# Kernel tuning notes

Measured on AMD Instinct MI355X. Metric: run time of the kernel, lower is better.

The kernel has to match this reference:

```python
import jax, jax.numpy as jnp
import numpy as np

B, C, J, L = 8, 256, 16, 256
NB_CODE = 8192
S_SCALES = [1, 2, 4, 8, 16]
T_SCALES = [4, 16, 64, 128, 256]
PHI_IDX = [0, 1, 1, 2, 3]   # si/(SN-1) mapped onto PhiPartiallyShared ticks (K=4)
RESI = 0.5                  # quant_resi
BETA = 1.0


def setup_inputs() -> dict:
    key = jax.random.key(0)
    k1, k2, k3 = jax.random.split(key, 3)
    return {
        "f_bcjl": jax.random.normal(k1, (B, C, J, L), jnp.float32),
        "codebook": jax.random.normal(k2, (NB_CODE, C), jnp.float32),
        "phi_w": jax.random.normal(k3, (4, C, C, 3, 3), jnp.float32) * (1.0 / np.sqrt(C * 9)),
        "phi_b": jnp.zeros((4, C), jnp.float32),
    }


def _area_down(x, sn, tn):
    # F.interpolate(mode='area') with divisible sizes == mean pooling
    b, c, j, l = x.shape
    return x.reshape(b, c, sn, j // sn, tn, l // tn).mean(axis=(3, 5))


def _cubic_w(x, a=-0.75):
    # PyTorch bicubic kernel (a = -0.75)
    ax = jnp.abs(x)
    w1 = ((a + 2.0) * ax - (a + 3.0)) * ax * ax + 1.0
    w2 = a * (ax * ((ax - 5.0) * ax + 8.0) - 4.0)
    return jnp.where(ax <= 1.0, w1, jnp.where(ax < 2.0, w2, 0.0))


def _resize_cubic_axis(x, out_size, axis):
    x = jnp.moveaxis(x, axis, -1)
    n = x.shape[-1]
    scale = n / out_size
    coords = (jnp.arange(out_size, dtype=jnp.float32) + 0.5) * scale - 0.5
    i0 = jnp.floor(coords)
    t = coords - i0
    offs = jnp.arange(-1, 3)
    idx = jnp.clip(i0.astype(jnp.int32)[:, None] + offs, 0, n - 1)   # [out,4], border-clamped
    w = _cubic_w(t[:, None] - offs.astype(jnp.float32))              # [out,4]
    g = x[..., idx]                                                  # [...,out,4]
    y = jnp.einsum('...ok,ok->...o', g, w)
    return jnp.moveaxis(y, -1, axis)


def _up_bicubic(x, j, l):
    return _resize_cubic_axis(_resize_cubic_axis(x, j, 2), l, 3)


def _phi(h, w, b):
    y = jax.lax.conv_general_dilated(h, w, (1, 1), ((1, 1), (1, 1)),
                                     dimension_numbers=('NCHW', 'OIHW', 'NCHW'))
    y = y + b[None, :, None, None]
    return h * (1.0 - RESI) + y * RESI


def _forward(f, cb, pw, pb):
    f_ng = jax.lax.stop_gradient(f)
    f_rest = f_ng
    f_hat = jnp.zeros_like(f_ng)
    loss = jnp.float32(0.0)
    idx_all = []
    SN = len(S_SCALES)
    cb_sq = jnp.sum(cb * cb, axis=1)  # [nb_code]
    for si, (sn, tn) in enumerate(zip(S_SCALES, T_SCALES)):
        r = f_rest if si == SN - 1 else _area_down(f_rest, sn, tn)
        rest = r.transpose(0, 2, 3, 1).reshape(-1, C)                     # [N,C]
        d = jnp.sum(rest * rest, axis=1, keepdims=True) + cb_sq - 2.0 * (rest @ cb.T)
        idx = jnp.argmin(d, axis=-1)                                      # eval-mode gumbel_sample == argmax(-d)
        idx_all.append(idx)
        h = cb[idx].reshape(-1, sn, tn, C).transpose(0, 3, 1, 2)          # [B,C,sn,tn]
        if si != SN - 1:
            h = _up_bicubic(h, J, L)
        h = _phi(h, pw[PHI_IDX[si]], pb[PHI_IDX[si]])
        f_hat = f_hat + h
        f_rest = f_rest - h
        loss = loss + BETA * jnp.mean((jax.lax.stop_gradient(f_hat) - f) ** 2)
    loss = loss / SN
    f_hat_out = f_hat - f_ng + f   # straight-through estimator
    return f_hat_out, loss, jnp.concatenate(idx_all)


def _perplexity(idx):
    counts = jnp.zeros((NB_CODE,), jnp.float32).at[idx].add(1.0)
    prob = counts / jnp.sum(counts)
    return jnp.exp(-jnp.sum(prob * jnp.log(prob + 1e-7)))


def reference(f_bcjl, codebook, phi_w, phi_b):
    f_hat, loss, idx = _forward(f_bcjl, codebook, phi_w, phi_b)
    return f_hat, loss, _perplexity(idx)
```

## Files before the change

### kernel.cpp

```cpp
#include <hip/hip_runtime.h>
#include <stdint.h>

#define BB 8
#define CC 256
#define JJ 16
#define LL 256
#define NPIX 32768
#define NEL (BB*CC*JJ*LL)
#define NBC 8192
#define NTOT 43296

typedef unsigned short u16;
typedef short short8 __attribute__((ext_vector_type(8)));
typedef float floatx4 __attribute__((ext_vector_type(4)));

__device__ __forceinline__ uint32_t ord_f32(float f) {
  uint32_t u = __float_as_uint(f);
  return (u & 0x80000000u) ? ~u : (u | 0x80000000u);
}

__device__ __forceinline__ float cubw(float x) {
  const float a = -0.75f;
  float ax = fabsf(x);
  if (ax <= 1.f) return ((a + 2.f) * ax - (a + 3.f)) * ax * ax + 1.f;
  if (ax < 2.f)  return a * (ax * ((ax - 5.f) * ax + 8.f) - 4.f);
  return 0.f;
}

__device__ __forceinline__ u16 bf16h(float x) {
  uint32_t u = __float_as_uint(x);
  return (u16)((u + 0x7FFFu + ((u >> 16) & 1u)) >> 16);
}
__device__ __forceinline__ float bf16f(u16 h) {
  return __uint_as_float(((uint32_t)h) << 16);
}

__global__ void k_init(unsigned long long* __restrict__ bkey,
                       uint32_t* __restrict__ counts, float* __restrict__ lacc) {
  int i = blockIdx.x * 256 + threadIdx.x;
  int stride = gridDim.x * 256;
  for (int x = i; x < NTOT; x += stride) bkey[x] = 0xFFFFFFFFFFFFFFFFull;
  for (int x = i; x < NBC; x += stride) counts[x] = 0u;
  if (i < 8) lacc[i] = 0.f;
}

__global__ void k_f2pm(const float* __restrict__ f, float* __restrict__ pm) {
  __shared__ float t[64][65];
  int tid = threadIdx.x;
  int px0 = blockIdx.x * 64, c0 = blockIdx.y * 64;
  int b = px0 >> 12, y = (px0 >> 8) & 15, x0 = px0 & 255;
#pragma unroll
  for (int it = 0; it < 4; ++it) {
    int slot = it * 256 + tid;
    int c = slot >> 4, q = (slot & 15) * 4;
    float4 v = *(const float4*)(f + (((size_t)(b * 256 + c0 + c)) * 16 + y) * 256 + x0 + q);
    t[c][q] = v.x; t[c][q + 1] = v.y; t[c][q + 2] = v.z; t[c][q + 3] = v.w;
  }
  __syncthreads();
#pragma unroll
  for (int it = 0; it < 4; ++it) {
    int slot = it * 256 + tid;
    int i = slot >> 4, q = (slot & 15) * 4;
    float4 v;
    v.x = t[q + 0][i]; v.y = t[q + 1][i]; v.z = t[q + 2][i]; v.w = t[q + 3][i];
    *(float4*)(pm + (size_t)(px0 + i) * 256 + c0 + q) = v;
  }
}

__global__ void k_out(const float* __restrict__ f, const float* __restrict__ pm,
                      float* __restrict__ out) {
  __shared__ float t[64][65];
  int tid = threadIdx.x;
  int px0 = blockIdx.x * 64, c0 = blockIdx.y * 64;
  int b = px0 >> 12, y = (px0 >> 8) & 15, x0 = px0 & 255;
#pragma unroll
  for (int it = 0; it < 4; ++it) {
    int slot = it * 256 + tid;
    int i = slot >> 4, q = (slot & 15) * 4;
    float4 v = *(const float4*)(pm + (size_t)(px0 + i) * 256 + c0 + q);
    t[q + 0][i] = v.x; t[q + 1][i] = v.y; t[q + 2][i] = v.z; t[q + 3][i] = v.w;
  }
  __syncthreads();
#pragma unroll
  for (int it = 0; it < 4; ++it) {
    int slot = it * 256 + tid;
    int c = slot >> 4, q = (slot & 15) * 4;
    size_t g = (((size_t)(b * 256 + c0 + c)) * 16 + y) * 256 + x0 + q;
    float4 fv = *(const float4*)(f + g);
    float4 o;
    o.x = fv.x - t[c][q + 0]; o.y = fv.y - t[c][q + 1];
    o.z = fv.z - t[c][q + 2]; o.w = fv.w - t[c][q + 3];
    *(float4*)(out + g) = o;
  }
}

__global__ void k_cbsq(const float* __restrict__ cb, float* __restrict__ cbsq) {
  int k = blockIdx.x * blockDim.x + threadIdx.x;
  if (k >= NBC) return;
  const float4* row = (const float4*)(cb + (size_t)k * CC);
  float s = 0.f;
  for (int i = 0; i < CC / 4; ++i) {
    float4 v = row[i];
    s += v.x * v.x + v.y * v.y + v.z * v.z + v.w * v.w;
  }
  cbsq[k] = s;
}

__global__ void k_split(const float* __restrict__ src, u16* __restrict__ hi,
                        u16* __restrict__ lo, int n) {
  int i = (blockIdx.x * 256 + threadIdx.x) * 4;
  if (i >= n) return;
  float4 v = *(const float4*)(src + i);
  ushort4 h, l;
  h.x = bf16h(v.x); l.x = bf16h(v.x - bf16f(h.x));
  h.y = bf16h(v.y); l.y = bf16h(v.y - bf16f(h.y));
  h.z = bf16h(v.z); l.z = bf16h(v.z - bf16f(h.z));
  h.w = bf16h(v.w); l.w = bf16h(v.w - bf16f(h.w));
  *(ushort4*)(hi + i) = h;
  *(ushort4*)(lo + i) = l;
}

__global__ void k_wprep(const float* __restrict__ pw, u16* __restrict__ Whi,
                        u16* __restrict__ Wlo) {
  int bx = blockIdx.x;
  int co = bx & 255;
  int ps = bx >> 8;
  int phi = ps / 9, s = ps % 9;
  int ci = threadIdx.x;
  float v = pw[(((size_t)(phi * 256 + co)) * 256 + ci) * 9 + s];
  u16 h = bf16h(v);
  Whi[(size_t)bx * 256 + ci] = h;
  Wlo[(size_t)bx * 256 + ci] = bf16h(v - bf16f(h));
}

__global__ void k_poolpart(const float* __restrict__ pm, float* __restrict__ part,
                           int sn, int tn, int pj, int wl, int K, int ppk) {
  int n = blockIdx.x, kk = blockIdx.y, c = threadIdx.x;
  int b = n / (sn * tn);
  int s = (n / tn) % sn;
  int t = n % tn;
  float acc = 0.f;
  for (int q = kk * ppk; q < (kk + 1) * ppk; ++q) {
    int yy = s * pj + q / wl;
    int xx = t * wl + q % wl;
    size_t p = (size_t)b * 4096 + (size_t)yy * 256 + xx;
    acc += pm[p * 256 + c];
  }
  part[((size_t)n * K + kk) * 256 + c] = acc;
}

__global__ void k_poolfin(const float* __restrict__ part, float* __restrict__ rows,
                          int K, float inv) {
  int n = blockIdx.x, c = threadIdx.x;
  float s = 0.f;
  for (int kk = 0; kk < K; ++kk) s += part[((size_t)n * K + kk) * 256 + c];
  rows[(size_t)n * 256 + c] = s * inv;
}

#define MS_QB 256
__global__ __launch_bounds__(512, 2) void k_msearch(
    const float* __restrict__ Q,
    const u16* __restrict__ CBhi, const u16* __restrict__ CBlo,
    const float* __restrict__ cbsq, unsigned long long* __restrict__ bkey,
    int nQ, int tilesPerBlock) {
  __shared__ __align__(16) u16 Bh[32 * 264];
  __shared__ __align__(16) u16 Bl[32 * 264];
  __shared__ float sq[32];
  int tid = threadIdx.x;
  int wid = tid >> 6, lane = tid & 63;
  int lm = lane & 15, quad = lane >> 4;
  int qw = blockIdx.x * MS_QB + wid * 32;
  int t0 = blockIdx.y * tilesPerBlock;

  short8 qh[2][8], ql[2][8];
#pragma unroll
  for (int mt = 0; mt < 2; ++mt)
#pragma unroll
    for (int kc = 0; kc < 8; ++kc) {
      const float* qp = Q + (size_t)(qw + mt * 16 + lm) * 256 + kc * 32 + quad * 8;
      float4 a = *(const float4*)qp;
      float4 b = *(const float4*)(qp + 4);
      float v[8] = {a.x, a.y, a.z, a.w, b.x, b.y, b.z, b.w};
      short8 h, l;
#pragma unroll
      for (int e = 0; e < 8; ++e) {
        u16 hh = bf16h(v[e]);
        h[e] = (short)hh;
        l[e] = (short)bf16h(v[e] - bf16f(hh));
      }
      qh[mt][kc] = h;
      ql[mt][kc] = l;
    }

  unsigned long long rk[2][4];
#pragma unroll
  for (int mt = 0; mt < 2; ++mt)
#pragma unroll
    for (int r = 0; r < 4; ++r) rk[mt][r] = 0xFFFFFFFFFFFFFFFFull;

  for (int t = 0; t < tilesPerBlock; ++t) {
    int n0 = (t0 + t) * 32;
    __syncthreads();
#pragma unroll
    for (int it = 0; it < 2; ++it) {
      int slot = tid + it * 512;
      int n = slot >> 5, ks = (slot & 31) * 8;
      *(uint4*)&Bh[n * 264 + ks] = *(const uint4*)(CBhi + (size_t)(n0 + n) * 256 + ks);
      *(uint4*)&Bl[n * 264 + ks] = *(const uint4*)(CBlo + (size_t)(n0 + n) * 256 + ks);
    }
    if (tid < 32) sq[tid] = cbsq[n0 + tid];
    __syncthreads();
#pragma unroll
    for (int nt = 0; nt < 2; ++nt) {
      floatx4 acc0 = {0.f, 0.f, 0.f, 0.f}, acc1 = {0.f, 0.f, 0.f, 0.f};
#pragma unroll
      for (int kc = 0; kc < 8; ++kc) {
        short8 bh = *(const short8*)&Bh[(nt * 16 + lm) * 264 + kc * 32 + quad * 8];
        short8 bl = *(const short8*)&Bl[(nt * 16 + lm) * 264 + kc * 32 + quad * 8];
        acc0 = __builtin_amdgcn_mfma_f32_16x16x32_bf16(qh[0][kc], bh, acc0, 0, 0, 0);
        acc0 = __builtin_amdgcn_mfma_f32_16x16x32_bf16(qh[0][kc], bl, acc0, 0, 0, 0);
        acc0 = __builtin_amdgcn_mfma_f32_16x16x32_bf16(ql[0][kc], bh, acc0, 0, 0, 0);
        acc1 = __builtin_amdgcn_mfma_f32_16x16x32_bf16(qh[1][kc], bh, acc1, 0, 0, 0);
        acc1 = __builtin_amdgcn_mfma_f32_16x16x32_bf16(qh[1][kc], bl, acc1, 0, 0, 0);
        acc1 = __builtin_amdgcn_mfma_f32_16x16x32_bf16(ql[1][kc], bh, acc1, 0, 0, 0);
      }
      uint32_t code = (uint32_t)(n0 + nt * 16 + lm);
      float csq = sq[nt * 16 + lm];
#pragma unroll
      for (int r = 0; r < 4; ++r) {
        float d0 = csq - 2.f * acc0[r];
        float d1 = csq - 2.f * acc1[r];
        unsigned long long k0 = ((unsigned long long)ord_f32(d0) << 32) | code;
        unsigned long long k1 = ((unsigned long long)ord_f32(d1) << 32) | code;
        if (k0 < rk[0][r]) rk[0][r] = k0;
        if (k1 < rk[1][r]) rk[1][r] = k1;
      }
    }
  }

#pragma unroll
  for (int mt = 0; mt < 2; ++mt)
#pragma unroll
    for (int r = 0; r < 4; ++r) {
      unsigned long long k = rk[mt][r];
#pragma unroll
      for (int off = 1; off <= 8; off <<= 1) {
        uint32_t lo = (uint32_t)k, hi = (uint32_t)(k >> 32);
        uint32_t olo = __shfl_xor(lo, off, 64);
        uint32_t ohi = __shfl_xor(hi, off, 64);
        unsigned long long ok = ((unsigned long long)ohi << 32) | olo;
        if (ok < k) k = ok;
      }
      if (lm == 0) {
        int q = qw + mt * 16 + quad * 4 + r;
        if (q < nQ) atomicMin(&bkey[q], k);
      }
    }
}

__global__ void k_upgather(const unsigned long long* __restrict__ bkey,
                           const float* __restrict__ cb,
                           u16* __restrict__ Hhi, u16* __restrict__ Hlo,
                           int sn, int tn, int last) {
  __shared__ int sidx[8][16];
  __shared__ float swgt[8][16];
  int tid = threadIdx.x;
  int p0 = blockIdx.x * 8;
  if (!last) {
    if (tid < 128) {
      int pp = tid >> 4, tap = tid & 15;
      int aa = tap >> 2, ee = tap & 3;
      int p = p0 + pp;
      int b = p >> 12, y = (p >> 8) & 15, x = p & 255;
      float cj = (y + 0.5f) * ((float)sn / 16.f) - 0.5f;
      float fj = floorf(cj); float tj = cj - fj; int ij = (int)fj;
      float wj = cubw(tj - (float)(aa - 1));
      int xj = min(max(ij + aa - 1, 0), sn - 1);
      float cl = (x + 0.5f) * ((float)tn / 256.f) - 0.5f;
      float fl = floorf(cl); float tl = cl - fl; int il = (int)fl;
      float wle = cubw(tl - (float)(ee - 1));
      int xl = min(max(il + ee - 1, 0), tn - 1);
      int n = (b * sn + xj) * tn + xl;
      sidx[pp][tap] = (int)((uint32_t)bkey[n] & (NBC - 1));
      swgt[pp][tap] = wj * wle;
    }
  } else {
    if (tid < 8) sidx[tid][0] = (int)((uint32_t)bkey[p0 + tid] & (NBC - 1));
  }
  __syncthreads();
  int c = tid;
  for (int pp = 0; pp < 8; ++pp) {
    float val;
    if (last) {
      val = cb[(size_t)sidx[pp][0] * 256 + c];
    } else {
      val = 0.f;
#pragma unroll
      for (int tap = 0; tap < 16; ++tap)
        val += swgt[pp][tap] * cb[(size_t)sidx[pp][tap] * 256 + c];
    }
    u16 h = bf16h(val);
    u16 l = bf16h(val - bf16f(h));
    size_t g = (size_t)(p0 + pp) * 256 + c;
    Hhi[g] = h;
    Hlo[g] = l;
  }
}

__global__ __launch_bounds__(256) void k_conv(
    const u16* __restrict__ Hhi, const u16* __restrict__ Hlo,
    const u16* __restrict__ Wh, const u16* __restrict__ Wl,
    const float* __restrict__ bias, float* __restrict__ pm,
    float* __restrict__ lacc, int si) {
  __shared__ __align__(16) u16 Ah[128 * 40];
  __shared__ __align__(16) u16 Al[128 * 40];
  __shared__ __align__(16) u16 Bh[128 * 40];
  __shared__ __align__(16) u16 Bl[128 * 40];
  __shared__ float redl[4];
  int tid = threadIdx.x;
  int mt = blockIdx.x >> 1, nt = blockIdx.x & 1;
  int px0 = mt * 128;
  int b4096 = px0 & ~4095;
  int y = (px0 >> 8) & 15;
  int x0 = px0 & 255;
  int co0 = nt * 128;
  int wid = tid >> 6, lane = tid & 63;
  int wm = wid & 1, wn = wid >> 1;
  int lm = lane & 15, quad = lane >> 4, k0 = quad * 8;

  floatx4 acc[4][4];
#pragma unroll
  for (int i = 0; i < 4; ++i)
#pragma unroll
    for (int j = 0; j < 4; ++j) acc[i][j] = (floatx4){0.f, 0.f, 0.f, 0.f};

  for (int s = 0; s < 9; ++s) {
    int dy = s / 3 - 1, dx = s % 3 - 1;
    int ys = y + dy;
    if (ys < 0 || ys > 15) continue;
    const u16* wbh = Wh + (size_t)s * 65536;
    const u16* wbl = Wl + (size_t)s * 65536;
    for (int ci0 = 0; ci0 < 256; ci0 += 32) {
      __syncthreads();
#pragma unroll
      for (int it = 0; it < 2; ++it) {
        int slot = tid + it * 256;
        int pxl = slot >> 2, ch = (slot & 3) * 8;
        int xs = x0 + pxl + dx;
        uint4 vh = {0, 0, 0, 0}, vl = {0, 0, 0, 0};
        if (xs >= 0 && xs < 256) {
          size_t g = ((size_t)(b4096 + ys * 256 + xs)) * 256 + ci0 + ch;
          vh = *(const uint4*)(Hhi + g);
          vl = *(const uint4*)(Hlo + g);
        }
        *(uint4*)&Ah[pxl * 40 + ch] = vh;
        *(uint4*)&Al[pxl * 40 + ch] = vl;
        size_t gw = (size_t)(co0 + pxl) * 256 + ci0 + ch;
        *(uint4*)&Bh[pxl * 40 + ch] = *(const uint4*)(wbh + gw);
        *(uint4*)&Bl[pxl * 40 + ch] = *(const uint4*)(wbl + gw);
      }
      __syncthreads();
      short8 ah[4], al[4], bh[4], bl[4];
#pragma unroll
      for (int mi = 0; mi < 4; ++mi) {
        int r = wm * 64 + mi * 16 + lm;
        ah[mi] = *(const short8*)&Ah[r * 40 + k0];
        al[mi] = *(const short8*)&Al[r * 40 + k0];
      }
#pragma unroll
      for (int ni = 0; ni < 4; ++ni) {
        int r = wn * 64 + ni * 16 + lm;
        bh[ni] = *(const short8*)&Bh[r * 40 + k0];
        bl[ni] = *(const short8*)&Bl[r * 40 + k0];
      }
#pragma unroll
      for (int mi = 0; mi < 4; ++mi)
#pragma unroll
        for (int ni = 0; ni < 4; ++ni) {
          acc[mi][ni] = __builtin_amdgcn_mfma_f32_16x16x32_bf16(ah[mi], bh[ni], acc[mi][ni], 0, 0, 0);
          acc[mi][ni] = __builtin_amdgcn_mfma_f32_16x16x32_bf16(ah[mi], bl[ni], acc[mi][ni], 0, 0, 0);
          acc[mi][ni] = __builtin_amdgcn_mfma_f32_16x16x32_bf16(al[mi], bh[ni], acc[mi][ni], 0, 0, 0);
        }
    }
  }

  float lsum = 0.f;
#pragma unroll
  for (int mi = 0; mi < 4; ++mi) {
#pragma unroll
    for (int ni = 0; ni < 4; ++ni) {
      int co = co0 + wn * 64 + ni * 16 + lm;
      float bv = bias[co];
#pragma unroll
      for (int r = 0; r < 4; ++r) {
        int px = px0 + wm * 64 + mi * 16 + quad * 4 + r;
        size_t g = (size_t)px * 256 + co;
        float h = bf16f(Hhi[g]) + bf16f(Hlo[g]);
        float o = 0.5f * h + 0.5f * (acc[mi][ni][r] + bv);
        float fr = pm[g] - o;
        pm[g] = fr;
        lsum += fr * fr;
      }
    }
  }
  for (int off = 32; off; off >>= 1) lsum += __shfl_xor(lsum, off, 64);
  if (lane == 0) redl[wid] = lsum;
  __syncthreads();
  if (tid == 0) atomicAdd(&lacc[si], redl[0] + redl[1] + redl[2] + redl[3]);
}

__global__ void k_hist(const unsigned long long* __restrict__ bkey,
                       uint32_t* __restrict__ counts) {
  int i = blockIdx.x * 256 + threadIdx.x;
  if (i < NTOT) atomicAdd(&counts[(uint32_t)bkey[i] & (NBC - 1)], 1u);
}

__global__ void k_scalars(const uint32_t* __restrict__ counts,
                          const float* __restrict__ lacc,
                          float* __restrict__ out) {
  __shared__ float red[4];
  int tid = threadIdx.x;
  float s = 0.f;
  for (int i = tid; i < NBC; i += 256) {
    float p = (float)counts[i] * (1.0f / (float)NTOT);
    s += p * logf(p + 1e-7f);
  }
  for (int off = 32; off; off >>= 1) s += __shfl_xor(s, off, 64);
  if ((tid & 63) == 0) red[tid >> 6] = s;
  __syncthreads();
  if (tid == 0) {
    float ent = red[0] + red[1] + red[2] + red[3];
    out[NEL + 1] = expf(-ent);
    float l = 0.f;
    for (int i = 0; i < 5; ++i) l += lacc[i];
    out[NEL] = l * (1.0f / (float)NEL / 5.0f);
  }
}

extern "C" void kernel_launch(void* const* d_in, const int* in_sizes, int n_in,
                              void* d_out, int out_size, void* d_ws, size_t ws_size,
                              hipStream_t stream) {
  const float* f  = (const float*)d_in[0];
  const float* cb = (const float*)d_in[1];
  const float* pw = (const float*)d_in[2];
  const float* pb = (const float*)d_in[3];
  float* out = (float*)d_out;

  char* ws = (char*)d_ws;
  size_t off = 0;
  auto alloc = [&](size_t bytes) {
    void* p = ws + off;
    off += (bytes + 255) & ~(size_t)255;
    return p;
  };
  float* pm    = (float*)alloc((size_t)NEL * 4);
  u16*   Hhi   = (u16*)alloc((size_t)NEL * 2);
  u16*   Hlo   = (u16*)alloc((size_t)NEL * 2);
  float* rows  = (float*)alloc((size_t)8192 * 256 * 4);
  float* part  = (float*)alloc((size_t)8192 * 256 * 4);
  u16*   Whi   = (u16*)alloc((size_t)4 * 9 * 65536 * 2);
  u16*   Wlo   = (u16*)alloc((size_t)4 * 9 * 65536 * 2);
  u16*   CBhi  = (u16*)alloc((size_t)NBC * 256 * 2);
  u16*   CBlo  = (u16*)alloc((size_t)NBC * 256 * 2);
  float* cbsq  = (float*)alloc((size_t)NBC * 4);
  unsigned long long* bkey = (unsigned long long*)alloc((size_t)NTOT * 8);
  uint32_t* counts = (uint32_t*)alloc((size_t)NBC * 4);
  float* lacc = (float*)alloc(8 * 4);

  k_init<<<256, 256, 0, stream>>>(bkey, counts, lacc);
  k_f2pm<<<dim3(NPIX / 64, 4), 256, 0, stream>>>(f, pm);
  k_cbsq<<<NBC / 256, 256, 0, stream>>>(cb, cbsq);
  k_split<<<(NBC * 256) / 1024, 256, 0, stream>>>(cb, CBhi, CBlo, NBC * 256);
  k_wprep<<<4 * 9 * 256, 256, 0, stream>>>(pw, Whi, Wlo);

  const int SNs[5]   = {1, 2, 4, 8, 16};
  const int TNs[5]   = {4, 16, 64, 128, 256};
  const int PHI[5]   = {0, 1, 1, 2, 3};
  const int KCH[5]   = {64, 64, 64, 16, 4};
  const int Ks[5]    = {16, 8, 2, 1, 1};
  int offs = 0;
  for (int si = 0; si < 5; ++si) {
    int sn = SNs[si], tn = TNs[si];
    int N = BB * sn * tn;
    int pj = JJ / sn, wl = LL / tn;
    unsigned long long* bk = bkey + offs;
    const float* qsrc;
    if (si < 4) {
      int K = Ks[si], npx = pj * wl;
      k_poolpart<<<dim3(N, K), 256, 0, stream>>>(pm, part, sn, tn, pj, wl, K, npx / K);
      k_poolfin<<<N, 256, 0, stream>>>(part, rows, K, 1.0f / (float)npx);
      qsrc = rows;
    } else {
      qsrc = pm;
    }
    int qtiles = (N + MS_QB - 1) / MS_QB;
    int tpb = (NBC / 32) / KCH[si];
    dim3 g(qtiles, KCH[si]);
    k_msearch<<<g, 512, 0, stream>>>(qsrc, CBhi, CBlo, cbsq, bk, N, tpb);
    k_upgather<<<NPIX / 8, 256, 0, stream>>>(bk, cb, Hhi, Hlo, sn, tn, si == 4);
    k_conv<<<512, 256, 0, stream>>>(Hhi, Hlo,
                                    Whi + (size_t)PHI[si] * 9 * 65536,
                                    Wlo + (size_t)PHI[si] * 9 * 65536,
                                    pb + (size_t)PHI[si] * 256, pm, lacc, si);
    offs += N;
  }
  k_hist<<<(NTOT + 255) / 256, 256, 0, stream>>>(bkey, counts);
  k_out<<<dim3(NPIX / 64, 4), 256, 0, stream>>>(f, pm, out);
  k_scalars<<<1, 256, 0, stream>>>(counts, lacc, out);
}
```

Before: 1.630 ms.

## Double-buffer codebook tiles in nearest-code search with MFMA-ordered LDS layout

Rewrites the codebook search kernel to double-buffer codebook tiles in shared memory. The next tile is prefetched into registers while MFMAs run on the current one, cutting the per-tile barrier pair to a single barrier. The tile is stored in LDS already permuted into MFMA fragment order so each lane reads one contiguous 16-byte chunk without padding. Blocks shrink to 256 threads and 128 queries, and the codebook split counts per scale are retuned, which adds more partial argmin blocks and raises register pressure from the prefetch buffers.

After: 1.996 ms. 1.22x slower.

```diff
diff --git a/kernel.cpp b/kernel.cpp
--- a/kernel.cpp
+++ b/kernel.cpp
@@ -157,20 +157,28 @@
   rows[(size_t)n * 256 + c] = s * inv;
 }
 
-#define MS_QB 256
-__global__ __launch_bounds__(512, 2) void k_msearch(
+#define MS_QB 128
+__global__ __launch_bounds__(256, 2) void k_msearch(
     const float* __restrict__ Q,
     const u16* __restrict__ CBhi, const u16* __restrict__ CBlo,
     const float* __restrict__ cbsq, unsigned long long* __restrict__ bkey,
     int nQ, int tilesPerBlock) {
-  __shared__ __align__(16) u16 Bh[32 * 264];
-  __shared__ __align__(16) u16 Bl[32 * 264];
-  __shared__ float sq[32];
+  __shared__ __align__(16) u16 Bh[2][32 * 256];
+  __shared__ __align__(16) u16 Bl[2][32 * 256];
+  __shared__ float sq[2][32];
   int tid = threadIdx.x;
   int wid = tid >> 6, lane = tid & 63;
   int lm = lane & 15, quad = lane >> 4;
   int qw = blockIdx.x * MS_QB + wid * 32;
   int t0 = blockIdx.y * tilesPerBlock;
+
+  int goff[4];
+#pragma unroll
+  for (int c = 0; c < 4; ++c) {
+    int lin = tid + c * 256;
+    int l4 = lin & 15, q4 = (lin >> 4) & 3, nt = (lin >> 6) & 1, kc = lin >> 7;
+    goff[c] = (nt * 16 + l4) * 256 + kc * 32 + q4 * 8;
+  }
 
   short8 qh[2][8], ql[2][8];
 #pragma unroll
@@ -198,25 +206,49 @@
 #pragma unroll
     for (int r = 0; r < 4; ++r) rk[mt][r] = 0xFFFFFFFFFFFFFFFFull;
 
+  {
+    size_t n0b = (size_t)t0 * 32 * 256;
+    float sv = (tid < 32) ? cbsq[t0 * 32 + tid] : 0.f;
+    uint4 rh[4], rl[4];
+#pragma unroll
+    for (int c = 0; c < 4; ++c) {
+      rh[c] = *(const uint4*)(CBhi + n0b + goff[c]);
+      rl[c] = *(const uint4*)(CBlo + n0b + goff[c]);
+    }
+#pragma unroll
+    for (int c = 0; c < 4; ++c) {
+      int lin = tid + c * 256;
+      *(uint4*)&Bh[0][lin * 8] = rh[c];
+      *(uint4*)&Bl[0][lin * 8] = rl[c];
+    }
+    if (tid < 32) sq[0][tid] = sv;
+  }
+  __syncthreads();
+
   for (int t = 0; t < tilesPerBlock; ++t) {
+    int p = t & 1;
+    bool pre = (t + 1 < tilesPerBlock);
+    uint4 rh[4], rl[4];
+    float sv = 0.f;
+    if (pre) {
+      int n1 = (t0 + t + 1) * 32;
+      size_t n1b = (size_t)n1 * 256;
+      if (tid < 32) sv = cbsq[n1 + tid];
+#pragma unroll
+      for (int c = 0; c < 4; ++c) {
+        rh[c] = *(const uint4*)(CBhi + n1b + goff[c]);
+        rl[c] = *(const uint4*)(CBlo + n1b + goff[c]);
+      }
+    }
     int n0 = (t0 + t) * 32;
-    __syncthreads();
-#pragma unroll
-    for (int it = 0; it < 2; ++it) {
-      int slot = tid + it * 512;
-      int n = slot >> 5, ks = (slot & 31) * 8;
-      *(uint4*)&Bh[n * 264 + ks] = *(const uint4*)(CBhi + (size_t)(n0 + n) * 256 + ks);
-      *(uint4*)&Bl[n * 264 + ks] = *(const uint4*)(CBlo + (size_t)(n0 + n) * 256 + ks);
-    }
-    if (tid < 32) sq[tid] = cbsq[n0 + tid];
-    __syncthreads();
 #pragma unroll
     for (int nt = 0; nt < 2; ++nt) {
       floatx4 acc0 = {0.f, 0.f, 0.f, 0.f}, acc1 = {0.f, 0.f, 0.f, 0.f};
 #pragma unroll
       for (int kc = 0; kc < 8; ++kc) {
-        short8 bh = *(const short8*)&Bh[(nt * 16 + lm) * 264 + kc * 32 + quad * 8];
-        short8 bl = *(const short8*)&Bl[(nt * 16 + lm) * 264 + kc * 32 + quad * 8];
+        int lb = ((kc * 2 + nt) * 64 + lane) * 8;
+        short8 bh = *(const short8*)&Bh[p][lb];
+        short8 bl = *(const short8*)&Bl[p][lb];
         acc0 = __builtin_amdgcn_mfma_f32_16x16x32_bf16(qh[0][kc], bh, acc0, 0, 0, 0);
         acc0 = __builtin_amdgcn_mfma_f32_16x16x32_bf16(qh[0][kc], bl, acc0, 0, 0, 0);
         acc0 = __builtin_amdgcn_mfma_f32_16x16x32_bf16(ql[0][kc], bh, acc0, 0, 0, 0);
@@ -225,7 +257,7 @@
         acc1 = __builtin_amdgcn_mfma_f32_16x16x32_bf16(ql[1][kc], bh, acc1, 0, 0, 0);
       }
       uint32_t code = (uint32_t)(n0 + nt * 16 + lm);
-      float csq = sq[nt * 16 + lm];
+      float csq = sq[p][nt * 16 + lm];
 #pragma unroll
       for (int r = 0; r < 4; ++r) {
         float d0 = csq - 2.f * acc0[r];
@@ -235,6 +267,16 @@
         if (k0 < rk[0][r]) rk[0][r] = k0;
         if (k1 < rk[1][r]) rk[1][r] = k1;
       }
+    }
+    if (pre) {
+#pragma unroll
+      for (int c = 0; c < 4; ++c) {
+        int lin = tid + c * 256;
+        *(uint4*)&Bh[p ^ 1][lin * 8] = rh[c];
+        *(uint4*)&Bl[p ^ 1][lin * 8] = rl[c];
+      }
+      if (tid < 32) sq[p ^ 1][tid] = sv;
+      __syncthreads();
     }
   }
 
@@ -476,7 +518,7 @@
   const int SNs[5]   = {1, 2, 4, 8, 16};
   const int TNs[5]   = {4, 16, 64, 128, 256};
   const int PHI[5]   = {0, 1, 1, 2, 3};
-  const int KCH[5]   = {64, 64, 64, 16, 4};
+  const int KCH[5]   = {256, 128, 32, 8, 2};
   const int Ks[5]    = {16, 8, 2, 1, 1};
   int offs = 0;
   for (int si = 0; si < 5; ++si) {
@@ -496,7 +538,7 @@
     int qtiles = (N + MS_QB - 1) / MS_QB;
     int tpb = (NBC / 32) / KCH[si];
     dim3 g(qtiles, KCH[si]);
-    k_msearch<<<g, 512, 0, stream>>>(qsrc, CBhi, CBlo, cbsq, bk, N, tpb);
+    k_msearch<<<g, 256, 0, stream>>>(qsrc, CBhi, CBlo, cbsq, bk, N, tpb);
     k_upgather<<<NPIX / 8, 256, 0, stream>>>(bk, cb, Hhi, Hlo, sn, tn, si == 4);
     k_conv<<<512, 256, 0, stream>>>(Hhi, Hlo,
                                     Whi + (size_t)PHI[si] * 9 * 65536,
```

## Double-buffer codebook tiles in LDS via async global loads in MFMA fragment layout

Applied to the files above, without the earlier changes.

The codebook hi/lo split is now written in MFMA-fragment order by a new prep kernel. The nearest-code search kernel loads each 32-code tile straight into LDS with global_load_lds and double-buffers it, so the next tile is fetched while the current one is computed. Per-tile squared norms are read directly from global memory instead of being staged in LDS. Block size drops to 256 threads with 128 queries per block, and the codebook split counts per scale are retuned to keep the grid filled. This targets the synchronous LDS staging and the two barriers per tile in the search loop, at the cost of more LDS per block and more partial-result atomics.

Result: faster. 1.565 ms (-4.0%).

```diff
diff --git a/kernel.cpp b/kernel.cpp
--- a/kernel.cpp
+++ b/kernel.cpp
@@ -33,6 +33,13 @@
 }
 __device__ __forceinline__ float bf16f(u16 h) {
   return __uint_as_float(((uint32_t)h) << 16);
+}
+
+__device__ __forceinline__ void gload_lds16(const void* g, void* l) {
+  __builtin_amdgcn_global_load_lds(
+      (__attribute__((address_space(1))) void*)g,
+      (__attribute__((address_space(3))) void*)(uint32_t)(uintptr_t)l,
+      16, 0, 0);
 }
 
 __global__ void k_init(unsigned long long* __restrict__ bkey,
@@ -106,18 +113,35 @@
   cbsq[k] = s;
 }
 
-__global__ void k_split(const float* __restrict__ src, u16* __restrict__ hi,
-                        u16* __restrict__ lo, int n) {
-  int i = (blockIdx.x * 256 + threadIdx.x) * 4;
-  if (i >= n) return;
-  float4 v = *(const float4*)(src + i);
-  ushort4 h, l;
-  h.x = bf16h(v.x); l.x = bf16h(v.x - bf16f(h.x));
-  h.y = bf16h(v.y); l.y = bf16h(v.y - bf16f(h.y));
-  h.z = bf16h(v.z); l.z = bf16h(v.z - bf16f(h.z));
-  h.w = bf16h(v.w); l.w = bf16h(v.w - bf16f(h.w));
-  *(ushort4*)(hi + i) = h;
-  *(ushort4*)(lo + i) = l;
+__global__ void k_cbprep(const float* __restrict__ cb, u16* __restrict__ fmh,
+                         u16* __restrict__ fml) {
+  int gid = blockIdx.x * 256 + threadIdx.x;
+  int t = gid >> 10, lin = gid & 1023;
+  int kcnt = lin >> 6;
+  int kc = kcnt >> 1, nt = kcnt & 1;
+  int lane = lin & 63;
+  int lm = lane & 15, quad = lane >> 4;
+  int code = t * 32 + nt * 16 + lm;
+  int k = kc * 32 + quad * 8;
+  const float* s = cb + (size_t)code * 256 + k;
+  float4 a = *(const float4*)s;
+  float4 b = *(const float4*)(s + 4);
+  float v[8] = {a.x, a.y, a.z, a.w, b.x, b.y, b.z, b.w};
+  ushort4 h0, h1, l0, l1;
+  u16 hh[8], ll[8];
+#pragma unroll
+  for (int e = 0; e < 8; ++e) {
+    hh[e] = bf16h(v[e]);
+    ll[e] = bf16h(v[e] - bf16f(hh[e]));
+  }
+  h0 = make_ushort4(hh[0], hh[1], hh[2], hh[3]);
+  h1 = make_ushort4(hh[4], hh[5], hh[6], hh[7]);
+  l0 = make_ushort4(ll[0], ll[1], ll[2], ll[3]);
+  l1 = make_ushort4(ll[4], ll[5], ll[6], ll[7]);
+  *(ushort4*)(fmh + (size_t)gid * 8) = h0;
+  *(ushort4*)(fmh + (size_t)gid * 8 + 4) = h1;
+  *(ushort4*)(fml + (size_t)gid * 8) = l0;
+  *(ushort4*)(fml + (size_t)gid * 8 + 4) = l1;
 }
 
 __global__ void k_wprep(const float* __restrict__ pw, u16* __restrict__ Whi,
@@ -157,20 +181,20 @@
   rows[(size_t)n * 256 + c] = s * inv;
 }
 
-#define MS_QB 256
-__global__ __launch_bounds__(512, 2) void k_msearch(
+#define MS_QB 128
+__global__ __launch_bounds__(256, 2) void k_msearch(
     const float* __restrict__ Q,
-    const u16* __restrict__ CBhi, const u16* __restrict__ CBlo,
+    const u16* __restrict__ FH, const u16* __restrict__ FL,
     const float* __restrict__ cbsq, unsigned long long* __restrict__ bkey,
     int nQ, int tilesPerBlock) {
-  __shared__ __align__(16) u16 Bh[32 * 264];
-  __shared__ __align__(16) u16 Bl[32 * 264];
-  __shared__ float sq[32];
+  __shared__ __align__(16) u16 Bh[2][8192];
+  __shared__ __align__(16) u16 Bl[2][8192];
   int tid = threadIdx.x;
   int wid = tid >> 6, lane = tid & 63;
   int lm = lane & 15, quad = lane >> 4;
   int qw = blockIdx.x * MS_QB + wid * 32;
   int t0 = blockIdx.y * tilesPerBlock;
+  int blane = wid * 4096 + lane * 16;
 
   short8 qh[2][8], ql[2][8];
 #pragma unroll
@@ -198,25 +222,40 @@
 #pragma unroll
     for (int r = 0; r < 4; ++r) rk[mt][r] = 0xFFFFFFFFFFFFFFFFull;
 
+  {
+    const char* sh = (const char*)FH + (size_t)t0 * 16384;
+    const char* sl = (const char*)FL + (size_t)t0 * 16384;
+#pragma unroll
+    for (int i = 0; i < 4; ++i) {
+      gload_lds16(sh + blane + i * 1024, (char*)&Bh[0][0] + wid * 4096 + i * 1024);
+      gload_lds16(sl + blane + i * 1024, (char*)&Bl[0][0] + wid * 4096 + i * 1024);
+    }
+  }
+  __syncthreads();
+
   for (int t = 0; t < tilesPerBlock; ++t) {
+    int p = t & 1;
+    bool pre = (t + 1 < tilesPerBlock);
+    if (pre) {
+      const char* sh = (const char*)FH + (size_t)(t0 + t + 1) * 16384;
+      const char* sl = (const char*)FL + (size_t)(t0 + t + 1) * 16384;
+#pragma unroll
+      for (int i = 0; i < 4; ++i) {
+        gload_lds16(sh + blane + i * 1024, (char*)&Bh[p ^ 1][0] + wid * 4096 + i * 1024);
+        gload_lds16(sl + blane + i * 1024, (char*)&Bl[p ^ 1][0] + wid * 4096 + i * 1024);
+      }
+    }
     int n0 = (t0 + t) * 32;
-    __syncthreads();
-#pragma unroll
-    for (int it = 0; it < 2; ++it) {
-      int slot = tid + it * 512;
-      int n = slot >> 5, ks = (slot & 31) * 8;
-      *(uint4*)&Bh[n * 264 + ks] = *(const uint4*)(CBhi + (size_t)(n0 + n) * 256 + ks);
-      *(uint4*)&Bl[n * 264 + ks] = *(const uint4*)(CBlo + (size_t)(n0 + n) * 256 + ks);
-    }
-    if (tid < 32) sq[tid] = cbsq[n0 + tid];
-    __syncthreads();
+    float csq0 = cbsq[n0 + lm];
+    float csq1 = cbsq[n0 + 16 + lm];
 #pragma unroll
     for (int nt = 0; nt < 2; ++nt) {
       floatx4 acc0 = {0.f, 0.f, 0.f, 0.f}, acc1 = {0.f, 0.f, 0.f, 0.f};
 #pragma unroll
       for (int kc = 0; kc < 8; ++kc) {
-        short8 bh = *(const short8*)&Bh[(nt * 16 + lm) * 264 + kc * 32 + quad * 8];
-        short8 bl = *(const short8*)&Bl[(nt * 16 + lm) * 264 + kc * 32 + quad * 8];
+        int lb = (kc * 2 + nt) * 512 + lane * 8;
+        short8 bh = *(const short8*)&Bh[p][lb];
+        short8 bl = *(const short8*)&Bl[p][lb];
         acc0 = __builtin_amdgcn_mfma_f32_16x16x32_bf16(qh[0][kc], bh, acc0, 0, 0, 0);
         acc0 = __builtin_amdgcn_mfma_f32_16x16x32_bf16(qh[0][kc], bl, acc0, 0, 0, 0);
         acc0 = __builtin_amdgcn_mfma_f32_16x16x32_bf16(ql[0][kc], bh, acc0, 0, 0, 0);
@@ -225,7 +264,7 @@
         acc1 = __builtin_amdgcn_mfma_f32_16x16x32_bf16(ql[1][kc], bh, acc1, 0, 0, 0);
       }
       uint32_t code = (uint32_t)(n0 + nt * 16 + lm);
-      float csq = sq[nt * 16 + lm];
+      float csq = nt ? csq1 : csq0;
 #pragma unroll
       for (int r = 0; r < 4; ++r) {
         float d0 = csq - 2.f * acc0[r];
@@ -236,6 +275,7 @@
         if (k1 < rk[1][r]) rk[1][r] = k1;
       }
     }
+    if (pre) __syncthreads();
   }
 
 #pragma unroll
@@ -460,8 +500,8 @@
   float* part  = (float*)alloc((size_t)8192 * 256 * 4);
   u16*   Whi   = (u16*)alloc((size_t)4 * 9 * 65536 * 2);
   u16*   Wlo   = (u16*)alloc((size_t)4 * 9 * 65536 * 2);
-  u16*   CBhi  = (u16*)alloc((size_t)NBC * 256 * 2);
-  u16*   CBlo  = (u16*)alloc((size_t)NBC * 256 * 2);
+  u16*   CBfh  = (u16*)alloc((size_t)NBC * 256 * 2);
+  u16*   CBfl  = (u16*)alloc((size_t)NBC * 256 * 2);
   float* cbsq  = (float*)alloc((size_t)NBC * 4);
   unsigned long long* bkey = (unsigned long long*)alloc((size_t)NTOT * 8);
   uint32_t* counts = (uint32_t*)alloc((size_t)NBC * 4);
@@ -470,13 +510,13 @@
   k_init<<<256, 256, 0, stream>>>(bkey, counts, lacc);
   k_f2pm<<<dim3(NPIX / 64, 4), 256, 0, stream>>>(f, pm);
   k_cbsq<<<NBC / 256, 256, 0, stream>>>(cb, cbsq);
-  k_split<<<(NBC * 256) / 1024, 256, 0, stream>>>(cb, CBhi, CBlo, NBC * 256);
+  k_cbprep<<<1024, 256, 0, stream>>>(cb, CBfh, CBfl);
   k_wprep<<<4 * 9 * 256, 256, 0, stream>>>(pw, Whi, Wlo);
 
   const int SNs[5]   = {1, 2, 4, 8, 16};
   const int TNs[5]   = {4, 16, 64, 128, 256};
   const int PHI[5]   = {0, 1, 1, 2, 3};
-  const int KCH[5]   = {64, 64, 64, 16, 4};
+  const int KCH[5]   = {256, 128, 32, 8, 2};
   const int Ks[5]    = {16, 8, 2, 1, 1};
   int offs = 0;
   for (int si = 0; si < 5; ++si) {
@@ -496,7 +536,7 @@
     int qtiles = (N + MS_QB - 1) / MS_QB;
     int tpb = (NBC / 32) / KCH[si];
     dim3 g(qtiles, KCH[si]);
-    k_msearch<<<g, 512, 0, stream>>>(qsrc, CBhi, CBlo, cbsq, bk, N, tpb);
+    k_msearch<<<g, 256, 0, stream>>>(qsrc, CBfh, CBfl, cbsq, bk, N, tpb);
     k_upgather<<<NPIX / 8, 256, 0, stream>>>(bk, cb, Hhi, Hlo, sn, tn, si == 4);
     k_conv<<<512, 256, 0, stream>>>(Hhi, Hlo,
                                     Whi + (size_t)PHI[si] * 9 * 65536,
```
